# Performance work log

Hardware: AMD Instinct MI355X
Metric: run time of the kernel (lower is better)

Reference implementation:

```python
import jax, jax.numpy as jnp
import numpy as np

EMBED_DIM = 1024
NUM_HEADS = 16
HEAD_DIM = EMBED_DIM // NUM_HEADS  # 64
ROPE_BASE = 10000.0


def _rope_cache(seq_len, dim):
    inv_freq = 1.0 / (ROPE_BASE ** (jnp.arange(0, dim, 2, dtype=jnp.float32) / dim))
    t = jnp.arange(seq_len, dtype=jnp.float32)
    freqs = jnp.einsum('i,j->ij', t, inv_freq)          # (T, D/2)
    emb = jnp.concatenate([freqs, freqs], axis=-1)      # (T, D)
    return jnp.cos(emb), jnp.sin(emb)


def _rotate_half(x):
    x1, x2 = x[..., : x.shape[-1] // 2], x[..., x.shape[-1] // 2:]
    return jnp.concatenate([-x2, x1], axis=-1)


def setup_inputs() -> dict:
    key = jax.random.key(0)
    k0, k1, k2 = jax.random.split(key, 3)
    B, T, C = 2, 2048, EMBED_DIM
    x = jax.random.normal(k0, (B, T, C), dtype=jnp.float32)
    # xavier-uniform-ish scale for qkv (fan_in=C, fan_out=3C) and out_proj
    lim_qkv = float(np.sqrt(6.0 / (C + 3 * C)))
    lim_out = float(np.sqrt(6.0 / (C + C)))
    Wqkv = jax.random.uniform(k1, (3 * C, C), jnp.float32, -lim_qkv, lim_qkv)
    Wout = jax.random.uniform(k2, (C, C), jnp.float32, -lim_out, lim_out)
    bout = jnp.zeros((C,), jnp.float32)
    attention_mask = jnp.ones((B, T), dtype=bool)
    return {"x": x, "Wqkv": Wqkv, "Wout": Wout, "bout": bout,
            "attention_mask": attention_mask}


def reference(x, Wqkv, Wout, bout, attention_mask):
    B, T, C = x.shape
    H, D = NUM_HEADS, HEAD_DIM
    scale = D ** -0.5

    qkv = jnp.einsum('btc,fc->btf', x, Wqkv)            # (B,T,3C)
    qkv = qkv.reshape(B, T, 3, H, D)
    q = qkv[:, :, 0].transpose(0, 2, 1, 3)              # (B,H,T,D)
    k = qkv[:, :, 1].transpose(0, 2, 1, 3)
    v = qkv[:, :, 2].transpose(0, 2, 1, 3)

    cos, sin = _rope_cache(T, D)                        # (T,D), broadcasts
    q = q * cos + _rotate_half(q) * sin
    k = k * cos + _rotate_half(k) * sin

    attn = jnp.einsum('bhqd,bhkd->bhqk', q, k) * scale  # (B,H,T,T)
    mask = (1.0 - attention_mask[:, None, None, :].astype(jnp.float32)) * -10000.0
    attn = jax.nn.softmax(attn + mask, axis=-1)
    attn = jnp.nan_to_num(attn, nan=1.0 / T)
    # dropout omitted (eval / dropout=0.0)

    out = jnp.einsum('bhqk,bhkd->bhqd', attn, v)        # (B,H,T,D)
    out = out.transpose(0, 2, 1, 3).reshape(B, T, C)
    return jnp.einsum('btc,oc->bto', out, Wout) + bout
```

## Files before the change

kernel.cpp:

```cpp
#include <hip/hip_runtime.h>
#include <math.h>

typedef __attribute__((ext_vector_type(8))) short short8;
typedef __attribute__((ext_vector_type(4))) float floatx4;

#define NB 2
#define SEQ 2048
#define NC 1024
#define NH 16
#define ND 64
#define NF 3072
#define NM 4096

__device__ __forceinline__ unsigned short f2bf(float f) {
  union { float f; unsigned u; } c; c.f = f;
  unsigned u = c.u;
  u += 0x7fffu + ((u >> 16) & 1u);
  return (unsigned short)(u >> 16);
}

__device__ __forceinline__ void gload16(const unsigned short* g, unsigned short* l) {
  __builtin_amdgcn_global_load_lds(
      (const __attribute__((address_space(1))) unsigned int*)g,
      (__attribute__((address_space(3))) unsigned int*)l, 16, 0, 0);
}

__device__ __forceinline__ int vperm64(int tl) {
  return (tl & 32) | (((tl >> 2) & 3) << 3) | (((tl >> 4) & 1) << 2) | (tl & 3);
}

#define R0 (NM * NC / 4)
#define R1 (NF * NC / 4)
#define R2 (NC * NC / 4)
#define RT (SEQ * 32)
__global__ __launch_bounds__(256) void cvt_all(const float* __restrict__ x,
                                               const float* __restrict__ wq,
                                               const float* __restrict__ wo,
                                               unsigned short* __restrict__ xb,
                                               unsigned short* __restrict__ wqb,
                                               unsigned short* __restrict__ wob,
                                               float2* __restrict__ tab) {
  int i = blockIdx.x * 256 + threadIdx.x;
  if (i >= R0 + R1 + R2) {
    int idx = i - (R0 + R1 + R2);
    int j = idx & 31, t = idx >> 5;
    float inv = exp2f((float)j * (-13.287712379549449f / 32.0f));
    float sn, cs;
    sincosf((float)t * inv, &sn, &cs);
    tab[idx] = make_float2(cs, sn);
    return;
  }
  const float* src;
  unsigned short* dst;
  int off;
  if (i < R0) { src = x; dst = xb; off = i; }
  else if (i < R0 + R1) { src = wq; dst = wqb; off = i - R0; }
  else { src = wo; dst = wob; off = i - R0 - R1; }
  float4 v = ((const float4*)src)[off];
  ushort4 r;
  r.x = f2bf(v.x); r.y = f2bf(v.y); r.z = f2bf(v.z); r.w = f2bf(v.w);
  ((ushort4*)dst)[off] = r;
}

template <int BN, int EPI>
__global__ __launch_bounds__(256) void gemm_m97(const unsigned short* __restrict__ A,
                                                const unsigned short* __restrict__ B,
                                                float* __restrict__ C,
                                                const float* __restrict__ bias,
                                                unsigned short* __restrict__ qb,
                                                unsigned short* __restrict__ kb,
                                                unsigned short* __restrict__ vt,
                                                const float2* __restrict__ tab,
                                                int M, int N, int K) {
  constexpr int NT = BN / 32;
  __shared__ __align__(16) unsigned short As[128 * 32];
  __shared__ __align__(16) unsigned short Bs[BN * 32];
  const int tid = threadIdx.x, lane = tid & 63, w = tid >> 6;
  const int g = lane & 15, q4 = lane >> 4;
  const int m0 = blockIdx.y * 128, n0 = blockIdx.x * BN;
  const int wm = (w & 1) * 64, wn = (w >> 1) * (BN / 2);
  floatx4 acc[4][NT];
#pragma unroll
  for (int i = 0; i < 4; i++)
#pragma unroll
    for (int j = 0; j < NT; j++) acc[i][j] = (floatx4)0.0f;
  const int lr = lane >> 2, lc = (lane & 3) * 8;
  const unsigned short* gA = A + (size_t)(m0 + w * 32 + lr) * K + lc;
  const unsigned short* gB = B + (size_t)(n0 + w * (BN / 4) + lr) * K + lc;
  unsigned short* lA0 = &As[(w * 32) * 32];
  unsigned short* lA1 = &As[(w * 32 + 16) * 32];
  unsigned short* lB0 = &Bs[(w * (BN / 4)) * 32];
  unsigned short* lB1 = &Bs[(w * (BN / 4) + 16) * 32];
  for (int k0 = 0; k0 < K; k0 += 32) {
    __syncthreads();
    gload16(gA + k0, lA0);
    gload16(gA + (size_t)16 * K + k0, lA1);
    gload16(gB + k0, lB0);
    if (BN == 128) gload16(gB + (size_t)16 * K + k0, lB1);
    __syncthreads();
    short8 af[4], bfr[NT];
#pragma unroll
    for (int mt = 0; mt < 4; mt++)
      af[mt] = *(const short8*)&As[(wm + mt * 16 + g) * 32 + q4 * 8];
#pragma unroll
    for (int nt = 0; nt < NT; nt++)
      bfr[nt] = *(const short8*)&Bs[(wn + nt * 16 + g) * 32 + q4 * 8];
#pragma unroll
    for (int mt = 0; mt < 4; mt++)
#pragma unroll
      for (int nt = 0; nt < NT; nt++)
        acc[mt][nt] = __builtin_amdgcn_mfma_f32_16x16x32_bf16(af[mt], bfr[nt], acc[mt][nt], 0, 0, 0);
  }
  if constexpr (EPI == 0) {
#pragma unroll
    for (int nt = 0; nt < NT; nt++) {
      const int col = n0 + wn + nt * 16 + g;
      const float bv = bias ? bias[col] : 0.0f;
#pragma unroll
      for (int mt = 0; mt < 4; mt++) {
        const int row = m0 + wm + mt * 16 + q4 * 4;
#pragma unroll
        for (int r = 0; r < 4; r++)
          C[(size_t)(row + r) * N + col] = acc[mt][nt][r] + bv;
      }
    }
  } else {
    const int sect = n0 >> 10;
    const int colbase = n0 + wn - sect * 1024;
    const int hh = colbase >> 6;
    if (sect < 2) {
      unsigned short* dst = (sect == 0) ? qb : kb;
#pragma unroll
      for (int np = 0; np < 2; np++) {
        const int j = np * 16 + g;
#pragma unroll
        for (int mt = 0; mt < 4; mt++) {
#pragma unroll
          for (int r = 0; r < 4; r++) {
            const int row = m0 + wm + mt * 16 + q4 * 4 + r;
            const int t = row & 2047, b = row >> 11;
            const float2 cs = tab[t * 32 + j];
            const float x1 = acc[mt][np][r], x2 = acc[mt][np + 2][r];
            const size_t o = (((size_t)(b * NH + hh)) * SEQ + t) * ND + j;
            dst[o]      = f2bf(x1 * cs.x - x2 * cs.y);
            dst[o + 32] = f2bf(x2 * cs.x + x1 * cs.y);
          }
        }
      }
    } else {
#pragma unroll
      for (int nt = 0; nt < 4; nt++) {
        const int d = nt * 16 + g;
#pragma unroll
        for (int mt = 0; mt < 4; mt++) {
#pragma unroll
          for (int r = 0; r < 4; r++) {
            const int row = m0 + wm + mt * 16 + q4 * 4 + r;
            const int t = row & 2047, b = row >> 11;
            const int tp = (t & ~63) | vperm64(t & 63);
            vt[(((size_t)(b * NH + hh)) * ND + d) * SEQ + tp] = f2bf(acc[mt][nt][r]);
          }
        }
      }
    }
  }
}

#define SCL 0.18033688011112042f

__global__ __launch_bounds__(256, 2) void attn_fwd3(const unsigned short* __restrict__ Qb,
                                                    const unsigned short* __restrict__ Kb,
                                                    const unsigned short* __restrict__ Vt,
                                                    unsigned short* __restrict__ Ob) {
  __shared__ __align__(16) unsigned short Ks[2][64 * 64];
  __shared__ __align__(16) unsigned short Vs[2][64 * 64];
  const int bid = blockIdx.x;
  const int qt = bid & 15, h = (bid >> 4) & 15, b = bid >> 8;
  const int bh = b * NH + h;
  const int tid = threadIdx.x, lane = tid & 63, wave = tid >> 6;
  const int g = lane & 15, q4 = lane >> 4;
  const size_t qrow = ((size_t)bh * SEQ + qt * 128 + wave * 32 + g) * ND;
  short8 qa00 = *(const short8*)(Qb + qrow + q4 * 8);
  short8 qa01 = *(const short8*)(Qb + qrow + 32 + q4 * 8);
  short8 qa10 = *(const short8*)(Qb + qrow + 16 * ND + q4 * 8);
  short8 qa11 = *(const short8*)(Qb + qrow + 16 * ND + 32 + q4 * 8);
  floatx4 oacc[2][4];
#pragma unroll
  for (int i = 0; i < 2; i++)
#pragma unroll
    for (int j = 0; j < 4; j++) oacc[i][j] = (floatx4)0.0f;
  float lsum0 = 0.0f, lsum1 = 0.0f;
  const unsigned short* kg = Kb + (size_t)bh * SEQ * ND + (size_t)(wave * 16 + (lane & 15)) * ND + (lane >> 4) * 8;
  const unsigned short* vg = Vt + (size_t)bh * ND * SEQ + (size_t)(wave * 16 + (lane & 15)) * SEQ + (lane >> 4) * 8;
  unsigned short* lk0[2] = {&Ks[0][wave * 1024], &Ks[1][wave * 1024]};
  unsigned short* lv0[2] = {&Vs[0][wave * 1024], &Vs[1][wave * 1024]};
  gload16(kg, lk0[0]);
  gload16(kg + 32, lk0[0] + 512);
  gload16(vg, lv0[0]);
  gload16(vg + 32, lv0[0] + 512);
  __syncthreads();
  for (int kt = 0; kt < 32; kt++) {
    const int cur = kt & 1;
    if (kt < 31) {
      const unsigned short* kp = kg + (size_t)(kt + 1) * 64 * ND;
      const unsigned short* vp = vg + (kt + 1) * 64;
      unsigned short* dk = lk0[cur ^ 1];
      unsigned short* dv = lv0[cur ^ 1];
      gload16(kp, dk);
      gload16(kp + 32, dk + 512);
      gload16(vp, dv);
      gload16(vp + 32, dv + 512);
    }
    floatx4 st0[4], st1[4];
#pragma unroll
    for (int nt = 0; nt < 4; nt++) {
      short8 kf0 = *(const short8*)&Ks[cur][nt * 1024 + q4 * 128 + g * 8];
      short8 kf1 = *(const short8*)&Ks[cur][nt * 1024 + 512 + q4 * 128 + g * 8];
      floatx4 z0 = (floatx4)0.0f, z1 = (floatx4)0.0f;
      z0 = __builtin_amdgcn_mfma_f32_16x16x32_bf16(kf0, qa00, z0, 0, 0, 0);
      z0 = __builtin_amdgcn_mfma_f32_16x16x32_bf16(kf1, qa01, z0, 0, 0, 0);
      z1 = __builtin_amdgcn_mfma_f32_16x16x32_bf16(kf0, qa10, z1, 0, 0, 0);
      z1 = __builtin_amdgcn_mfma_f32_16x16x32_bf16(kf1, qa11, z1, 0, 0, 0);
      st0[nt] = z0;
      st1[nt] = z1;
    }
    short8 va0[4], va1[4];
#pragma unroll
    for (int dt = 0; dt < 4; dt++) {
      va0[dt] = *(const short8*)&Vs[cur][dt * 1024 + q4 * 128 + g * 8];
      va1[dt] = *(const short8*)&Vs[cur][dt * 1024 + 512 + q4 * 128 + g * 8];
    }
    {
      uint pd[8];
#pragma unroll
      for (int nt = 0; nt < 4; nt++) {
#pragma unroll
        for (int u = 0; u < 2; u++) {
          float pe = __builtin_amdgcn_exp2f(st0[nt][2 * u] * SCL);
          float po = __builtin_amdgcn_exp2f(st0[nt][2 * u + 1] * SCL);
          lsum0 += pe + po;
          unsigned ue = __builtin_bit_cast(unsigned, pe) + 0x8000u;
          unsigned uo = __builtin_bit_cast(unsigned, po) + 0x8000u;
          pd[nt * 2 + u] = __builtin_amdgcn_perm(uo, ue, 0x07060302u);
        }
      }
      short8 B0 = {(short)pd[0], (short)(pd[0] >> 16), (short)pd[1], (short)(pd[1] >> 16),
                   (short)pd[2], (short)(pd[2] >> 16), (short)pd[3], (short)(pd[3] >> 16)};
      short8 B1 = {(short)pd[4], (short)(pd[4] >> 16), (short)pd[5], (short)(pd[5] >> 16),
                   (short)pd[6], (short)(pd[6] >> 16), (short)pd[7], (short)(pd[7] >> 16)};
#pragma unroll
      for (int dt = 0; dt < 4; dt++) {
        oacc[0][dt] = __builtin_amdgcn_mfma_f32_16x16x32_bf16(va0[dt], B0, oacc[0][dt], 0, 0, 0);
        oacc[0][dt] = __builtin_amdgcn_mfma_f32_16x16x32_bf16(va1[dt], B1, oacc[0][dt], 0, 0, 0);
      }
    }
    {
      uint pd[8];
#pragma unroll
      for (int nt = 0; nt < 4; nt++) {
#pragma unroll
        for (int u = 0; u < 2; u++) {
          float pe = __builtin_amdgcn_exp2f(st1[nt][2 * u] * SCL);
          float po = __builtin_amdgcn_exp2f(st1[nt][2 * u + 1] * SCL);
          lsum1 += pe + po;
          unsigned ue = __builtin_bit_cast(unsigned, pe) + 0x8000u;
          unsigned uo = __builtin_bit_cast(unsigned, po) + 0x8000u;
          pd[nt * 2 + u] = __builtin_amdgcn_perm(uo, ue, 0x07060302u);
        }
      }
      short8 B0 = {(short)pd[0], (short)(pd[0] >> 16), (short)pd[1], (short)(pd[1] >> 16),
                   (short)pd[2], (short)(pd[2] >> 16), (short)pd[3], (short)(pd[3] >> 16)};
      short8 B1 = {(short)pd[4], (short)(pd[4] >> 16), (short)pd[5], (short)(pd[5] >> 16),
                   (short)pd[6], (short)(pd[6] >> 16), (short)pd[7], (short)(pd[7] >> 16)};
#pragma unroll
      for (int dt = 0; dt < 4; dt++) {
        oacc[1][dt] = __builtin_amdgcn_mfma_f32_16x16x32_bf16(va0[dt], B0, oacc[1][dt], 0, 0, 0);
        oacc[1][dt] = __builtin_amdgcn_mfma_f32_16x16x32_bf16(va1[dt], B1, oacc[1][dt], 0, 0, 0);
      }
    }
    __syncthreads();
  }
  lsum0 += __shfl_xor(lsum0, 16, 64);
  lsum0 += __shfl_xor(lsum0, 32, 64);
  lsum1 += __shfl_xor(lsum1, 16, 64);
  lsum1 += __shfl_xor(lsum1, 32, 64);
  const float iv0 = 1.0f / lsum0;
  const float iv1 = 1.0f / lsum1;
  const int tq0 = qt * 128 + wave * 32 + g;
  unsigned short* ob0 = Ob + ((size_t)b * SEQ + tq0) * NC + h * ND + q4 * 4;
  unsigned short* ob1 = ob0 + (size_t)16 * NC;
#pragma unroll
  for (int dt = 0; dt < 4; dt++) {
    uint u0 = __builtin_bit_cast(unsigned, oacc[0][dt][0] * iv0) + 0x8000u;
    uint u1 = __builtin_bit_cast(unsigned, oacc[0][dt][1] * iv0) + 0x8000u;
    uint u2 = __builtin_bit_cast(unsigned, oacc[0][dt][2] * iv0) + 0x8000u;
    uint u3 = __builtin_bit_cast(unsigned, oacc[0][dt][3] * iv0) + 0x8000u;
    *(uint2*)(ob0 + dt * 16) = make_uint2(__builtin_amdgcn_perm(u1, u0, 0x07060302u),
                                          __builtin_amdgcn_perm(u3, u2, 0x07060302u));
    uint w0 = __builtin_bit_cast(unsigned, oacc[1][dt][0] * iv1) + 0x8000u;
    uint w1 = __builtin_bit_cast(unsigned, oacc[1][dt][1] * iv1) + 0x8000u;
    uint w2 = __builtin_bit_cast(unsigned, oacc[1][dt][2] * iv1) + 0x8000u;
    uint w3 = __builtin_bit_cast(unsigned, oacc[1][dt][3] * iv1) + 0x8000u;
    *(uint2*)(ob1 + dt * 16) = make_uint2(__builtin_amdgcn_perm(w1, w0, 0x07060302u),
                                          __builtin_amdgcn_perm(w3, w2, 0x07060302u));
  }
}

extern "C" void kernel_launch(void* const* d_in, const int* in_sizes, int n_in,
                              void* d_out, int out_size, void* d_ws, size_t ws_size,
                              hipStream_t stream) {
  const float* x    = (const float*)d_in[0];
  const float* Wqkv = (const float*)d_in[1];
  const float* Wout = (const float*)d_in[2];
  const float* bout = (const float*)d_in[3];
  float* out = (float*)d_out;

  char* ws = (char*)d_ws;
  unsigned short* xb    = (unsigned short*)ws;
  unsigned short* wqkvb = xb + (size_t)NM * NC;
  unsigned short* woutb = wqkvb + (size_t)NF * NC;
  unsigned short* qb    = woutb + (size_t)NC * NC;
  unsigned short* kb    = qb + (size_t)NM * NC;
  unsigned short* vt    = kb + (size_t)NM * NC;
  unsigned short* ob    = vt + (size_t)NM * NC;
  float2* tab           = (float2*)(ob + (size_t)NM * NC);

  cvt_all<<<(R0 + R1 + R2 + RT) / 256, 256, 0, stream>>>(x, Wqkv, Wout, xb, wqkvb, woutb, tab);
  gemm_m97<128, 1><<<dim3(NF / 128, NM / 128), 256, 0, stream>>>(
      xb, wqkvb, nullptr, nullptr, qb, kb, vt, tab, NM, NF, NC);
  attn_fwd3<<<NB * NH * (SEQ / 128), 256, 0, stream>>>(qb, kb, vt, ob);
  gemm_m97<64, 0><<<dim3(NC / 64, NM / 128), 256, 0, stream>>>(
      ob, woutb, out, bout, nullptr, nullptr, nullptr, nullptr, NM, NC, NC);
}
```

Measured before the change: 193.7 us.

## Split attention over key dimension with combine kernel, fold scale into Q, swizzle GEMM LDS

Attention now splits the key range in two, launching twice as many blocks with a higher occupancy hint. Each block writes unnormalized fp32 partial outputs and row sums, and a new combine kernel adds them, normalizes and converts to bf16. The softmax scale moves into the Q epilogue of the QKV GEMM, and the GEMM shared-memory tile layout changes to a blocked arrangement meant to reduce bank conflicts. The split adds about 32MB of fp32 partial-output traffic plus an extra launch, in exchange for more parallelism (512 blocks instead of 256 on a many-CU device).

```diff
diff --git a/kernel.cpp b/kernel.cpp
--- a/kernel.cpp
+++ b/kernel.cpp
@@ -11,6 +11,9 @@
 #define ND 64
 #define NF 3072
 #define NM 4096
+#define KSPLIT 2
+
+#define SCL 0.18033688011112042f
 
 __device__ __forceinline__ unsigned short f2bf(float f) {
   union { float f; unsigned u; } c; c.f = f;
@@ -84,13 +87,13 @@
   for (int i = 0; i < 4; i++)
 #pragma unroll
     for (int j = 0; j < NT; j++) acc[i][j] = (floatx4)0.0f;
-  const int lr = lane >> 2, lc = (lane & 3) * 8;
-  const unsigned short* gA = A + (size_t)(m0 + w * 32 + lr) * K + lc;
-  const unsigned short* gB = B + (size_t)(n0 + w * (BN / 4) + lr) * K + lc;
-  unsigned short* lA0 = &As[(w * 32) * 32];
-  unsigned short* lA1 = &As[(w * 32 + 16) * 32];
-  unsigned short* lB0 = &Bs[(w * (BN / 4)) * 32];
-  unsigned short* lB1 = &Bs[(w * (BN / 4) + 16) * 32];
+  const int sr = lane & 15, sc = (lane >> 4) * 8;
+  const unsigned short* gA = A + (size_t)(m0 + w * 32 + sr) * K + sc;
+  const unsigned short* gB = B + (size_t)(n0 + w * (BN / 4) + sr) * K + sc;
+  unsigned short* lA0 = &As[w * 1024];
+  unsigned short* lA1 = &As[w * 1024 + 512];
+  unsigned short* lB0 = (BN == 128) ? &Bs[w * 1024] : &Bs[w * 512];
+  unsigned short* lB1 = (BN == 128) ? &Bs[w * 1024 + 512] : nullptr;
   for (int k0 = 0; k0 < K; k0 += 32) {
     __syncthreads();
     gload16(gA + k0, lA0);
@@ -101,10 +104,10 @@
     short8 af[4], bfr[NT];
 #pragma unroll
     for (int mt = 0; mt < 4; mt++)
-      af[mt] = *(const short8*)&As[(wm + mt * 16 + g) * 32 + q4 * 8];
+      af[mt] = *(const short8*)&As[((wm >> 4) + mt) * 512 + q4 * 128 + g * 8];
 #pragma unroll
     for (int nt = 0; nt < NT; nt++)
-      bfr[nt] = *(const short8*)&Bs[(wn + nt * 16 + g) * 32 + q4 * 8];
+      bfr[nt] = *(const short8*)&Bs[((wn >> 4) + nt) * 512 + q4 * 128 + g * 8];
 #pragma unroll
     for (int mt = 0; mt < 4; mt++)
 #pragma unroll
@@ -130,6 +133,7 @@
     const int hh = colbase >> 6;
     if (sect < 2) {
       unsigned short* dst = (sect == 0) ? qb : kb;
+      const float postscale = (sect == 0) ? SCL : 1.0f;
 #pragma unroll
       for (int np = 0; np < 2; np++) {
         const int j = np * 16 + g;
@@ -142,8 +146,8 @@
             const float2 cs = tab[t * 32 + j];
             const float x1 = acc[mt][np][r], x2 = acc[mt][np + 2][r];
             const size_t o = (((size_t)(b * NH + hh)) * SEQ + t) * ND + j;
-            dst[o]      = f2bf(x1 * cs.x - x2 * cs.y);
-            dst[o + 32] = f2bf(x2 * cs.x + x1 * cs.y);
+            dst[o]      = f2bf((x1 * cs.x - x2 * cs.y) * postscale);
+            dst[o + 32] = f2bf((x2 * cs.x + x1 * cs.y) * postscale);
           }
         }
       }
@@ -166,16 +170,15 @@
   }
 }
 
-#define SCL 0.18033688011112042f
-
-__global__ __launch_bounds__(256, 2) void attn_fwd3(const unsigned short* __restrict__ Qb,
+__global__ __launch_bounds__(256, 4) void attn_fwd5(const unsigned short* __restrict__ Qb,
                                                     const unsigned short* __restrict__ Kb,
                                                     const unsigned short* __restrict__ Vt,
-                                                    unsigned short* __restrict__ Ob) {
+                                                    float* __restrict__ Op,
+                                                    float* __restrict__ Lp) {
   __shared__ __align__(16) unsigned short Ks[2][64 * 64];
   __shared__ __align__(16) unsigned short Vs[2][64 * 64];
   const int bid = blockIdx.x;
-  const int qt = bid & 15, h = (bid >> 4) & 15, b = bid >> 8;
+  const int ks = bid & 1, qt = (bid >> 1) & 15, h = (bid >> 5) & 15, b = bid >> 9;
   const int bh = b * NH + h;
   const int tid = threadIdx.x, lane = tid & 63, wave = tid >> 6;
   const int g = lane & 15, q4 = lane >> 4;
@@ -190,8 +193,9 @@
 #pragma unroll
     for (int j = 0; j < 4; j++) oacc[i][j] = (floatx4)0.0f;
   float lsum0 = 0.0f, lsum1 = 0.0f;
-  const unsigned short* kg = Kb + (size_t)bh * SEQ * ND + (size_t)(wave * 16 + (lane & 15)) * ND + (lane >> 4) * 8;
-  const unsigned short* vg = Vt + (size_t)bh * ND * SEQ + (size_t)(wave * 16 + (lane & 15)) * SEQ + (lane >> 4) * 8;
+  const int kq0 = ks * (SEQ / KSPLIT);
+  const unsigned short* kg = Kb + (size_t)bh * SEQ * ND + (size_t)(kq0 + wave * 16 + (lane & 15)) * ND + (lane >> 4) * 8;
+  const unsigned short* vg = Vt + (size_t)bh * ND * SEQ + (size_t)(wave * 16 + (lane & 15)) * SEQ + kq0 + (lane >> 4) * 8;
   unsigned short* lk0[2] = {&Ks[0][wave * 1024], &Ks[1][wave * 1024]};
   unsigned short* lv0[2] = {&Vs[0][wave * 1024], &Vs[1][wave * 1024]};
   gload16(kg, lk0[0]);
@@ -199,9 +203,10 @@
   gload16(vg, lv0[0]);
   gload16(vg + 32, lv0[0] + 512);
   __syncthreads();
-  for (int kt = 0; kt < 32; kt++) {
+  const int NIT = SEQ / KSPLIT / 64;
+  for (int kt = 0; kt < NIT; kt++) {
     const int cur = kt & 1;
-    if (kt < 31) {
+    if (kt < NIT - 1) {
       const unsigned short* kp = kg + (size_t)(kt + 1) * 64 * ND;
       const unsigned short* vp = vg + (kt + 1) * 64;
       unsigned short* dk = lk0[cur ^ 1];
@@ -236,8 +241,8 @@
       for (int nt = 0; nt < 4; nt++) {
 #pragma unroll
         for (int u = 0; u < 2; u++) {
-          float pe = __builtin_amdgcn_exp2f(st0[nt][2 * u] * SCL);
-          float po = __builtin_amdgcn_exp2f(st0[nt][2 * u + 1] * SCL);
+          float pe = __builtin_amdgcn_exp2f(st0[nt][2 * u]);
+          float po = __builtin_amdgcn_exp2f(st0[nt][2 * u + 1]);
           lsum0 += pe + po;
           unsigned ue = __builtin_bit_cast(unsigned, pe) + 0x8000u;
           unsigned uo = __builtin_bit_cast(unsigned, po) + 0x8000u;
@@ -260,8 +265,8 @@
       for (int nt = 0; nt < 4; nt++) {
 #pragma unroll
         for (int u = 0; u < 2; u++) {
-          float pe = __builtin_amdgcn_exp2f(st1[nt][2 * u] * SCL);
-          float po = __builtin_amdgcn_exp2f(st1[nt][2 * u + 1] * SCL);
+          float pe = __builtin_amdgcn_exp2f(st1[nt][2 * u]);
+          float po = __builtin_amdgcn_exp2f(st1[nt][2 * u + 1]);
           lsum1 += pe + po;
           unsigned ue = __builtin_bit_cast(unsigned, pe) + 0x8000u;
           unsigned uo = __builtin_bit_cast(unsigned, po) + 0x8000u;
@@ -284,26 +289,40 @@
   lsum0 += __shfl_xor(lsum0, 32, 64);
   lsum1 += __shfl_xor(lsum1, 16, 64);
   lsum1 += __shfl_xor(lsum1, 32, 64);
-  const float iv0 = 1.0f / lsum0;
-  const float iv1 = 1.0f / lsum1;
   const int tq0 = qt * 128 + wave * 32 + g;
-  unsigned short* ob0 = Ob + ((size_t)b * SEQ + tq0) * NC + h * ND + q4 * 4;
-  unsigned short* ob1 = ob0 + (size_t)16 * NC;
+  float* op = Op + (size_t)ks * NM * NC;
+  float* o0 = op + ((size_t)b * SEQ + tq0) * NC + h * ND + q4 * 4;
+  float* o1 = o0 + (size_t)16 * NC;
 #pragma unroll
   for (int dt = 0; dt < 4; dt++) {
-    uint u0 = __builtin_bit_cast(unsigned, oacc[0][dt][0] * iv0) + 0x8000u;
-    uint u1 = __builtin_bit_cast(unsigned, oacc[0][dt][1] * iv0) + 0x8000u;
-    uint u2 = __builtin_bit_cast(unsigned, oacc[0][dt][2] * iv0) + 0x8000u;
-    uint u3 = __builtin_bit_cast(unsigned, oacc[0][dt][3] * iv0) + 0x8000u;
-    *(uint2*)(ob0 + dt * 16) = make_uint2(__builtin_amdgcn_perm(u1, u0, 0x07060302u),
-                                          __builtin_amdgcn_perm(u3, u2, 0x07060302u));
-    uint w0 = __builtin_bit_cast(unsigned, oacc[1][dt][0] * iv1) + 0x8000u;
-    uint w1 = __builtin_bit_cast(unsigned, oacc[1][dt][1] * iv1) + 0x8000u;
-    uint w2 = __builtin_bit_cast(unsigned, oacc[1][dt][2] * iv1) + 0x8000u;
-    uint w3 = __builtin_bit_cast(unsigned, oacc[1][dt][3] * iv1) + 0x8000u;
-    *(uint2*)(ob1 + dt * 16) = make_uint2(__builtin_amdgcn_perm(w1, w0, 0x07060302u),
-                                          __builtin_amdgcn_perm(w3, w2, 0x07060302u));
-  }
+    *(float4*)(o0 + dt * 16) = make_float4(oacc[0][dt][0], oacc[0][dt][1], oacc[0][dt][2], oacc[0][dt][3]);
+    *(float4*)(o1 + dt * 16) = make_float4(oacc[1][dt][0], oacc[1][dt][1], oacc[1][dt][2], oacc[1][dt][3]);
+  }
+  if (q4 == 0) {
+    float* lp = Lp + (size_t)ks * NB * NH * SEQ + (size_t)bh * SEQ;
+    lp[tq0] = lsum0;
+    lp[tq0 + 16] = lsum1;
+  }
+}
+
+__global__ __launch_bounds__(256) void attn_cmb(const float* __restrict__ Op,
+                                                const float* __restrict__ Lp,
+                                                unsigned short* __restrict__ Ob) {
+  int i = blockIdx.x * 256 + threadIdx.x;
+  const int row = i >> 8;
+  const int c = (i & 255) * 4;
+  const int b = row >> 11, t = row & 2047, h = c >> 6;
+  const size_t lidx = (size_t)(b * NH + h) * SEQ + t;
+  const float l = Lp[lidx] + Lp[(size_t)NB * NH * SEQ + lidx];
+  const float iv = 1.0f / l;
+  float4 a = ((const float4*)Op)[i];
+  float4 d = ((const float4*)(Op + (size_t)NM * NC))[i];
+  ushort4 r;
+  r.x = f2bf((a.x + d.x) * iv);
+  r.y = f2bf((a.y + d.y) * iv);
+  r.z = f2bf((a.z + d.z) * iv);
+  r.w = f2bf((a.w + d.w) * iv);
+  ((ushort4*)Ob)[i] = r;
 }
 
 extern "C" void kernel_launch(void* const* d_in, const int* in_sizes, int n_in,
@@ -324,11 +343,14 @@
   unsigned short* vt    = kb + (size_t)NM * NC;
   unsigned short* ob    = vt + (size_t)NM * NC;
   float2* tab           = (float2*)(ob + (size_t)NM * NC);
+  float* Op             = (float*)(tab + SEQ * 32);
+  float* Lp             = Op + (size_t)KSPLIT * NM * NC;
 
   cvt_all<<<(R0 + R1 + R2 + RT) / 256, 256, 0, stream>>>(x, Wqkv, Wout, xb, wqkvb, woutb, tab);
   gemm_m97<128, 1><<<dim3(NF / 128, NM / 128), 256, 0, stream>>>(
       xb, wqkvb, nullptr, nullptr, qb, kb, vt, tab, NM, NF, NC);
-  attn_fwd3<<<NB * NH * (SEQ / 128), 256, 0, stream>>>(qb, kb, vt, ob);
+  attn_fwd5<<<NB * NH * (SEQ / 128) * KSPLIT, 256, 0, stream>>>(qb, kb, vt, Op, Lp);
+  attn_cmb<<<(NM * NC / 4) / 256, 256, 0, stream>>>(Op, Lp, ob);
   gemm_m97<64, 0><<<dim3(NC / 64, NM / 128), 256, 0, stream>>>(
       ob, woutb, out, bout, nullptr, nullptr, nullptr, nullptr, NM, NC, NC);
 }
```

Result: slower. 213.0 us (+10.0%).
